# Optimization experiments

Measured on AMD Instinct MI355X. Metric: run time of the kernel, lower is better.

Reference implementation:

```python
import jax, jax.numpy as jnp
import numpy as np

N_NODES = 50000
N_EDGES = 800000
C_IN = 64
N_HEADS = 4
HEAD_DIM = 16
FC = 64


def setup_inputs() -> dict:
    key = jax.random.key(0)
    ks = jax.random.split(key, 20)
    d = {}
    d["node_input"] = jax.random.normal(ks[0], (N_NODES, C_IN), jnp.float32)
    d["node_attr"] = jnp.ones((N_NODES, 1), jnp.float32)
    d["edge_src"] = jax.random.randint(ks[1], (N_EDGES,), 0, N_NODES)
    d["edge_dst"] = jax.random.randint(ks[2], (N_EDGES,), 0, N_NODES)
    d["edge_attr"] = jax.random.normal(ks[3], (N_EDGES, 1), jnp.float32)
    d["edge_scalars"] = jax.random.normal(ks[4], (N_EDGES, FC), jnp.float32)
    d["batch"] = jnp.zeros((N_NODES,), jnp.int32)
    s = 1.0 / np.sqrt(C_IN)
    AD = N_HEADS * HEAD_DIM  # 64
    d["Wq"] = jax.random.normal(ks[5], (C_IN, AD), jnp.float32) * s
    d["bq"] = jnp.zeros((AD,), jnp.float32)
    d["W_src"] = jax.random.normal(ks[6], (C_IN, C_IN), jnp.float32) * s
    d["b_src"] = jnp.zeros((C_IN,), jnp.float32)
    d["W_dst"] = jax.random.normal(ks[7], (C_IN, C_IN), jnp.float32) * s
    d["W_fc1"] = jax.random.normal(ks[8], (FC, FC), jnp.float32) * (1.0 / np.sqrt(FC))
    d["b_fc1"] = jnp.zeros((FC,), jnp.float32)
    d["W_fc2"] = jax.random.normal(ks[9], (FC, FC), jnp.float32) * (1.0 / np.sqrt(FC))
    d["b_fc2"] = jnp.zeros((FC,), jnp.float32)
    d["W_fc3"] = jax.random.normal(ks[10], (FC, C_IN), jnp.float32) * (1.0 / np.sqrt(FC))
    d["b_fc3"] = jnp.zeros((C_IN,), jnp.float32)
    d["W_kv"] = jax.random.normal(ks[11], (C_IN, 2 * AD), jnp.float32) * s
    d["b_kv"] = jnp.zeros((2 * AD,), jnp.float32)
    d["W_proj"] = jax.random.normal(ks[12], (AD, C_IN), jnp.float32) * (1.0 / np.sqrt(AD))
    d["b_proj"] = jnp.zeros((C_IN,), jnp.float32)
    return d


def reference(node_input, node_attr, edge_src, edge_dst, edge_attr, edge_scalars, batch,
              Wq, bq, W_src, b_src, W_dst, W_fc1, b_fc1, W_fc2, b_fc2, W_fc3, b_fc3,
              W_kv, b_kv, W_proj, b_proj):
    N = node_input.shape[0]
    # query: linear -> heads -> scale (ScaleFactor for HxH 0e irreps = 1/sqrt(num_irreps))
    q = (node_input @ Wq + bq).reshape(N, N_HEADS, HEAD_DIM)
    q = q * (1.0 / jnp.sqrt(jnp.float32(HEAD_DIM)))
    # edge messages
    msg_src = node_input @ W_src + b_src
    msg_dst = node_input @ W_dst
    kv = msg_src[edge_src] + msg_dst[edge_dst]  # [E, C]
    # SeparableFCTP (scalar irreps): radial MLP -> depthwise weights, x * edge_attr, linear
    h = jax.nn.silu(edge_scalars @ W_fc1 + b_fc1)
    h = jax.nn.silu(h @ W_fc2 + b_fc2)
    w = h @ W_fc3 + b_fc3  # [E, C] depthwise TP weights
    tp = kv * edge_attr * w
    kv2 = (tp @ W_kv + b_kv).reshape(-1, 2 * N_HEADS, HEAD_DIM)
    k = kv2[:, :N_HEADS]
    v = kv2[:, N_HEADS:]
    # per-edge scores and segment softmax over incoming edges of each dst node
    alpha = jnp.einsum('ehd,ehd->eh', q[edge_dst], k)  # [E, H]
    seg_max = jax.ops.segment_max(alpha, edge_dst, num_segments=N)
    seg_max = jnp.where(jnp.isfinite(seg_max), seg_max, 0.0)
    ex = jnp.exp(alpha - seg_max[edge_dst])
    denom = jax.ops.segment_sum(ex, edge_dst, num_segments=N)
    alpha = ex / (denom[edge_dst] + 1e-16)
    # weighted scatter-sum of values
    attn = jax.ops.segment_sum(v * alpha[..., None], edge_dst, num_segments=N)
    attn = attn.reshape(N, N_HEADS * HEAD_DIM)
    return attn @ W_proj + b_proj
```

## Files before the change

### kernel.cpp

```cpp
#include <hip/hip_runtime.h>
#include <hip/hip_bf16.h>


typedef __attribute__((ext_vector_type(8))) short    bf16x8;
typedef __attribute__((ext_vector_type(4))) float    f32x4;
typedef __attribute__((ext_vector_type(4))) unsigned short ushort4v;

__device__ __forceinline__ unsigned short f2bf(float x) {
    union { float f; unsigned u; } v; v.f = x;
    unsigned r = v.u + 0x7fffu + ((v.u >> 16) & 1u);
    return (unsigned short)(r >> 16);
}

__device__ __forceinline__ int swz(int row, int k) {
    return row * 64 + (k ^ ((row & 7) << 3));
}

__device__ __forceinline__ bf16x8 ldfrag(const unsigned short* buf, int rn, int kk, int lhi) {
    return *(const bf16x8*)(buf + swz(rn, kk * 32 + lhi * 8));
}

__global__ __launch_bounds__(256)
void prep_weights(const float* __restrict__ W1, const float* __restrict__ W2,
                  const float* __restrict__ W3, const float* __restrict__ Wkv,
                  unsigned short* __restrict__ wbf)
{
    const int d = blockIdx.x * 256 + threadIdx.x;
    if (d < 12288) {
        const int w  = d >> 12;
        const int r  = d & 4095;
        const int n  = r >> 6, kx = r & 63;
        const int k  = kx ^ ((n & 7) << 3);
        const float* W = (w == 0) ? W1 : (w == 1) ? W2 : W3;
        wbf[d] = f2bf(W[k * 64 + n]);
    } else if (d < 20480) {
        const int r  = d - 12288;
        const int n  = r >> 6, kx = r & 63;
        const int k  = kx ^ ((n & 7) << 3);
        wbf[d] = f2bf(Wkv[k * 128 + n]);
    }
}

__global__ __launch_bounds__(384)
void node_linear_kernel(const float* __restrict__ x,
                        const float* __restrict__ Wq,   const float* __restrict__ bq,
                        const float* __restrict__ Wsrc, const float* __restrict__ bsrc,
                        const float* __restrict__ Wdst,
                        float* __restrict__ qout, float* __restrict__ msout,
                        float* __restrict__ mdout, int N, int ntiles)
{
    __shared__ __align__(16) float sW[64 * 192];
    __shared__ float sb[192];
    __shared__ __align__(16) float xs[32][68];

    const int t = threadIdx.x;
    for (int idx4 = t; idx4 < 3072; idx4 += 384) {
        const int k  = idx4 / 48;
        const int j4 = idx4 % 48;
        const float4* src = (j4 < 16) ? (const float4*)&Wq  [k * 64 + j4 * 4]
                         : (j4 < 32) ? (const float4*)&Wsrc[k * 64 + (j4 - 16) * 4]
                                     : (const float4*)&Wdst[k * 64 + (j4 - 32) * 4];
        ((float4*)sW)[idx4] = *src;
    }
    if (t < 192) sb[t] = (t < 64) ? bq[t] : (t < 128) ? bsrc[t - 64] : 0.0f;

    const int te = t / 48, tj = t % 48;
    const int j0 = tj * 4, e0 = te * 4;

    for (int tile = blockIdx.x; tile < ntiles; tile += gridDim.x) {
        const int nbase = tile * 32;
        __syncthreads();
        for (int idx = t; idx < 512; idx += 384) {
            const int n  = idx >> 4;
            const int c4 = (idx & 15) * 4;
            const int gn = nbase + n;
            float4 g = make_float4(0.f, 0.f, 0.f, 0.f);
            if (gn < N) g = *(const float4*)&x[(size_t)gn * 64 + c4];
            *(float4*)&xs[n][c4] = g;
        }
        __syncthreads();

        float acc[4][4];
#pragma unroll
        for (int i = 0; i < 4; ++i)
#pragma unroll
            for (int c = 0; c < 4; ++c) acc[i][c] = 0.f;

#pragma unroll 16
        for (int k = 0; k < 64; ++k) {
            const float4 wv = *(const float4*)&sW[k * 192 + j0];
            const float a0 = xs[e0 + 0][k], a1 = xs[e0 + 1][k];
            const float a2 = xs[e0 + 2][k], a3 = xs[e0 + 3][k];
            acc[0][0] += a0 * wv.x; acc[0][1] += a0 * wv.y; acc[0][2] += a0 * wv.z; acc[0][3] += a0 * wv.w;
            acc[1][0] += a1 * wv.x; acc[1][1] += a1 * wv.y; acc[1][2] += a1 * wv.z; acc[1][3] += a1 * wv.w;
            acc[2][0] += a2 * wv.x; acc[2][1] += a2 * wv.y; acc[2][2] += a2 * wv.z; acc[2][3] += a2 * wv.w;
            acc[3][0] += a3 * wv.x; acc[3][1] += a3 * wv.y; acc[3][2] += a3 * wv.z; acc[3][3] += a3 * wv.w;
        }

#pragma unroll
        for (int i = 0; i < 4; ++i) {
            const int gn = nbase + e0 + i;
            if (gn >= N) continue;
            float4 o;
            o.x = acc[i][0] + sb[j0 + 0];
            o.y = acc[i][1] + sb[j0 + 1];
            o.z = acc[i][2] + sb[j0 + 2];
            o.w = acc[i][3] + sb[j0 + 3];
            if (j0 < 64) {
                o.x *= 0.25f; o.y *= 0.25f; o.z *= 0.25f; o.w *= 0.25f;
                *(float4*)&qout[(size_t)gn * 64 + j0] = o;
            } else if (j0 < 128) {
                *(float4*)&msout[(size_t)gn * 64 + (j0 - 64)] = o;
            } else {
                *(float4*)&mdout[(size_t)gn * 64 + (j0 - 128)] = o;
            }
        }
    }
}

__global__ __launch_bounds__(512, 4)
void edge_fused_mfma(const int* __restrict__ esrc, const int* __restrict__ edst,
                     const float* __restrict__ eattr, const float* __restrict__ escal,
                     const unsigned short* __restrict__ wbf,
                     const float* __restrict__ b1, const float* __restrict__ b2,
                     const float* __restrict__ b3, const float* __restrict__ bkv,
                     const float* __restrict__ qbuf, const float* __restrict__ msrc,
                     const float* __restrict__ mdst,
                     float* __restrict__ num, float* __restrict__ den, int ntiles)
{
    __shared__ __align__(16) unsigned short sh[36864];
    unsigned short* sW1t  = sh;
    unsigned short* sW2t  = sh + 4096;
    unsigned short* sW3t  = sh + 8192;
    unsigned short* sWkvt = sh + 12288;
    unsigned short* sA0   = sh + 20480;
    unsigned short* sA1   = sh + 28672;
    __shared__ float sB1[64], sB2[64], sB3[64], sBkv[128], sEa[128];
    __shared__ int   sSrc[128], sDst[128];

    const int t    = threadIdx.x;
    const int lane = t & 63;
    const int wave = t >> 6;
    const int l15  = lane & 15;
    const int lhi  = lane >> 4;
    const int rowBase = wave * 16;

    for (int i4 = t; i4 < 2560; i4 += 512)
        ((float4*)sh)[i4] = ((const float4*)wbf)[i4];
    if (t < 64)              { sB1[t] = b1[t]; sB2[t] = b2[t]; sB3[t] = b3[t]; }
    if (t >= 64 && t < 192)  sBkv[t - 64] = bkv[t - 64];

    for (int tile = blockIdx.x; tile < ntiles; tile += gridDim.x) {
        const int base = tile * 128;
        __syncthreads();

        {
            int e = t >> 4;
            const int c4 = (t & 15) << 2;
#pragma unroll
            for (int p = 0; p < 4; ++p, e += 32) {
                const float4 g = *(const float4*)&escal[(size_t)(base + e) * 64 + c4];
                ushort4v pk = { f2bf(g.x), f2bf(g.y), f2bf(g.z), f2bf(g.w) };
                *(ushort4v*)&sA0[swz(e, c4)] = pk;
            }
        }
        if (t >= 192 && t < 320) {
            const int e = t - 192;
            sSrc[e] = esrc[base + e];
            sDst[e] = edst[base + e];
            sEa[e]  = eattr[base + e];
        }
        __syncthreads();

        {
            f32x4 acc[4] = {{0,0,0,0},{0,0,0,0},{0,0,0,0},{0,0,0,0}};
#pragma unroll
            for (int kk = 0; kk < 2; ++kk) {
                const bf16x8 a = ldfrag(sA0, rowBase + l15, kk, lhi);
#pragma unroll
                for (int c = 0; c < 4; ++c) {
                    const bf16x8 b = ldfrag(sW1t, c * 16 + l15, kk, lhi);
                    acc[c] = __builtin_amdgcn_mfma_f32_16x16x32_bf16(a, b, acc[c], 0, 0, 0);
                }
            }
#pragma unroll
            for (int c = 0; c < 4; ++c)
#pragma unroll
                for (int r = 0; r < 4; ++r) {
                    const int row = rowBase + lhi * 4 + r;
                    const int col = c * 16 + l15;
                    const float v = acc[c][r] + sB1[col];
                    sA1[swz(row, col)] = f2bf(v / (1.f + __expf(-v)));
                }
        }
        __syncthreads();

        {
            f32x4 acc[4] = {{0,0,0,0},{0,0,0,0},{0,0,0,0},{0,0,0,0}};
#pragma unroll
            for (int kk = 0; kk < 2; ++kk) {
                const bf16x8 a = ldfrag(sA1, rowBase + l15, kk, lhi);
#pragma unroll
                for (int c = 0; c < 4; ++c) {
                    const bf16x8 b = ldfrag(sW2t, c * 16 + l15, kk, lhi);
                    acc[c] = __builtin_amdgcn_mfma_f32_16x16x32_bf16(a, b, acc[c], 0, 0, 0);
                }
            }
#pragma unroll
            for (int c = 0; c < 4; ++c)
#pragma unroll
                for (int r = 0; r < 4; ++r) {
                    const int row = rowBase + lhi * 4 + r;
                    const int col = c * 16 + l15;
                    const float v = acc[c][r] + sB2[col];
                    sA0[swz(row, col)] = f2bf(v / (1.f + __expf(-v)));
                }
        }
        __syncthreads();

        {
            f32x4 acc[4] = {{0,0,0,0},{0,0,0,0},{0,0,0,0},{0,0,0,0}};
#pragma unroll
            for (int kk = 0; kk < 2; ++kk) {
                const bf16x8 a = ldfrag(sA0, rowBase + l15, kk, lhi);
#pragma unroll
                for (int c = 0; c < 4; ++c) {
                    const bf16x8 b = ldfrag(sW3t, c * 16 + l15, kk, lhi);
                    acc[c] = __builtin_amdgcn_mfma_f32_16x16x32_bf16(a, b, acc[c], 0, 0, 0);
                }
            }
            float ms[4][4], md[4][4];
#pragma unroll
            for (int c = 0; c < 4; ++c)
#pragma unroll
                for (int r = 0; r < 4; ++r) {
                    const int row = rowBase + lhi * 4 + r;
                    const int col = c * 16 + l15;
                    ms[c][r] = msrc[(size_t)sSrc[row] * 64 + col];
                    md[c][r] = mdst[(size_t)sDst[row] * 64 + col];
                }
#pragma unroll
            for (int c = 0; c < 4; ++c)
#pragma unroll
                for (int r = 0; r < 4; ++r) {
                    const int row = rowBase + lhi * 4 + r;
                    const int col = c * 16 + l15;
                    const float w  = acc[c][r] + sB3[col];
                    const float tp = (ms[c][r] + md[c][r]) * sEa[row] * w;
                    sA1[swz(row, col)] = f2bf(tp);
                }
        }
        __syncthreads();

        f32x4 acc2[8] = {{0,0,0,0},{0,0,0,0},{0,0,0,0},{0,0,0,0},
                         {0,0,0,0},{0,0,0,0},{0,0,0,0},{0,0,0,0}};
#pragma unroll
        for (int kk = 0; kk < 2; ++kk) {
            const bf16x8 a = ldfrag(sA1, rowBase + l15, kk, lhi);
#pragma unroll
            for (int c = 0; c < 8; ++c) {
                const bf16x8 b = ldfrag(sWkvt, c * 16 + l15, kk, lhi);
                acc2[c] = __builtin_amdgcn_mfma_f32_16x16x32_bf16(a, b, acc2[c], 0, 0, 0);
            }
        }

        int   gds[4];
        float qreg[4][4];
#pragma unroll
        for (int r = 0; r < 4; ++r) gds[r] = sDst[rowBase + lhi * 4 + r];
#pragma unroll
        for (int h = 0; h < 4; ++h)
#pragma unroll
            for (int r = 0; r < 4; ++r)
                qreg[h][r] = qbuf[(size_t)gds[r] * 64 + h * 16 + l15];

        float ex[4][4];
#pragma unroll
        for (int h = 0; h < 4; ++h)
#pragma unroll
            for (int r = 0; r < 4; ++r) {
                float s = (acc2[h][r] + sBkv[h * 16 + l15]) * qreg[h][r];
                s += __shfl_xor(s, 1);
                s += __shfl_xor(s, 2);
                s += __shfl_xor(s, 4);
                s += __shfl_xor(s, 8);
                const float e = __expf(s);
                ex[h][r] = e;
                if (l15 == h * 4 + r) atomicAdd(&den[(size_t)gds[r] * 4 + h], e);
            }

#pragma unroll
        for (int vt = 0; vt < 4; ++vt)
#pragma unroll
            for (int r = 0; r < 4; ++r) {
                const float vv = acc2[4 + vt][r] + sBkv[64 + vt * 16 + l15];
                atomicAdd(&num[(size_t)gds[r] * 64 + vt * 16 + l15], ex[vt][r] * vv);
            }
    }
}

__global__ __launch_bounds__(256)
void final_proj_kernel(const float* __restrict__ num, const float* __restrict__ den,
                       const float* __restrict__ Wp, const float* __restrict__ bp,
                       float* __restrict__ out, int N, int ntiles)
{
    __shared__ __align__(16) float sW[64 * 64];
    __shared__ float sb[64];
    __shared__ __align__(16) float at[64][68];

    const int t = threadIdx.x;
    for (int i4 = t; i4 < 1024; i4 += 256)
        ((float4*)sW)[i4] = ((const float4*)Wp)[i4];
    if (t < 64) sb[t] = bp[t];

    const int te = t >> 4, tj = t & 15;
    const int j0 = tj * 4, e0 = te * 4;

    for (int tile = blockIdx.x; tile < ntiles; tile += gridDim.x) {
        const int nbase = tile * 64;
        __syncthreads();
        for (int idx = t; idx < 1024; idx += 256) {
            const int n  = idx >> 4;
            const int c4 = (idx & 15) * 4;
            const int gn = nbase + n;
            float4 g = make_float4(0.f, 0.f, 0.f, 0.f);
            if (gn < N) {
                const float4 nm = *(const float4*)&num[(size_t)gn * 64 + c4];
                const float inv = 1.0f / (den[(size_t)gn * 4 + (c4 >> 4)] + 1e-16f);
                g = make_float4(nm.x * inv, nm.y * inv, nm.z * inv, nm.w * inv);
            }
            *(float4*)&at[n][c4] = g;
        }
        __syncthreads();

        float acc[4][4];
#pragma unroll
        for (int i = 0; i < 4; ++i)
#pragma unroll
            for (int c = 0; c < 4; ++c) acc[i][c] = 0.f;

#pragma unroll 16
        for (int k = 0; k < 64; ++k) {
            const float4 wv = *(const float4*)&sW[k * 64 + j0];
            const float a0 = at[e0 + 0][k], a1 = at[e0 + 1][k];
            const float a2 = at[e0 + 2][k], a3 = at[e0 + 3][k];
            acc[0][0] += a0 * wv.x; acc[0][1] += a0 * wv.y; acc[0][2] += a0 * wv.z; acc[0][3] += a0 * wv.w;
            acc[1][0] += a1 * wv.x; acc[1][1] += a1 * wv.y; acc[1][2] += a1 * wv.z; acc[1][3] += a1 * wv.w;
            acc[2][0] += a2 * wv.x; acc[2][1] += a2 * wv.y; acc[2][2] += a2 * wv.z; acc[2][3] += a2 * wv.w;
            acc[3][0] += a3 * wv.x; acc[3][1] += a3 * wv.y; acc[3][2] += a3 * wv.z; acc[3][3] += a3 * wv.w;
        }

#pragma unroll
        for (int i = 0; i < 4; ++i) {
            const int gn = nbase + e0 + i;
            if (gn >= N) continue;
            float4 o;
            o.x = acc[i][0] + sb[j0 + 0];
            o.y = acc[i][1] + sb[j0 + 1];
            o.z = acc[i][2] + sb[j0 + 2];
            o.w = acc[i][3] + sb[j0 + 3];
            *(float4*)&out[(size_t)gn * 64 + j0] = o;
        }
    }
}

extern "C" void kernel_launch(void* const* d_in, const int* in_sizes, int n_in,
                              void* d_out, int out_size, void* d_ws, size_t ws_size,
                              hipStream_t stream)
{
    const float* node_input = (const float*)d_in[0];
    const int*   edge_src   = (const int*)  d_in[2];
    const int*   edge_dst   = (const int*)  d_in[3];
    const float* edge_attr  = (const float*)d_in[4];
    const float* edge_scal  = (const float*)d_in[5];
    const float* Wq    = (const float*)d_in[7];
    const float* bq    = (const float*)d_in[8];
    const float* W_src = (const float*)d_in[9];
    const float* b_src = (const float*)d_in[10];
    const float* W_dst = (const float*)d_in[11];
    const float* W_fc1 = (const float*)d_in[12];
    const float* b_fc1 = (const float*)d_in[13];
    const float* W_fc2 = (const float*)d_in[14];
    const float* b_fc2 = (const float*)d_in[15];
    const float* W_fc3 = (const float*)d_in[16];
    const float* b_fc3 = (const float*)d_in[17];
    const float* W_kv  = (const float*)d_in[18];
    const float* b_kv  = (const float*)d_in[19];
    const float* W_proj = (const float*)d_in[20];
    const float* b_proj = (const float*)d_in[21];

    const int N = in_sizes[0] / 64;
    const int E = in_sizes[2];

    float* ws    = (float*)d_ws;
    float* q_buf = ws;
    float* msrc  = ws + (size_t)N * 64;
    float* mdst  = ws + (size_t)N * 128;
    float* num   = ws + (size_t)N * 192;
    float* den   = ws + (size_t)N * 256;
    unsigned short* wbf = (unsigned short*)(ws + (size_t)N * 260);

    hipMemsetAsync(num, 0, (size_t)N * 68 * sizeof(float), stream);

    prep_weights<<<80, 256, 0, stream>>>(W_fc1, W_fc2, W_fc3, W_kv, wbf);

    {
        const int ntiles = (N + 31) / 32;
        node_linear_kernel<<<512, 384, 0, stream>>>(node_input, Wq, bq, W_src, b_src, W_dst,
                                                    q_buf, msrc, mdst, N, ntiles);
    }
    {
        const int ntiles = E / 128;
        edge_fused_mfma<<<512, 512, 0, stream>>>(edge_src, edge_dst, edge_attr, edge_scal,
                                                 wbf, b_fc1, b_fc2, b_fc3, b_kv,
                                                 q_buf, msrc, mdst, num, den, ntiles);
    }
    {
        const int ntiles = (N + 63) / 64;
        final_proj_kernel<<<512, 256, 0, stream>>>(num, den, W_proj, b_proj,
                                                   (float*)d_out, N, ntiles);
    }
}
```

Baseline: 672.2 us.

## Make edge tiles wave-private, drop block barriers, and prefetch query gathers

```diff
diff --git a/kernel.cpp b/kernel.cpp
--- a/kernel.cpp
+++ b/kernel.cpp
@@ -19,6 +19,8 @@
 __device__ __forceinline__ bf16x8 ldfrag(const unsigned short* buf, int rn, int kk, int lhi) {
     return *(const bf16x8*)(buf + swz(rn, kk * 32 + lhi * 8));
 }
+
+#define PHASE_FENCE() asm volatile("" ::: "memory")
 
 __global__ __launch_bounds__(256)
 void prep_weights(const float* __restrict__ W1, const float* __restrict__ W2,
@@ -135,8 +137,7 @@
     unsigned short* sWkvt = sh + 12288;
     unsigned short* sA0   = sh + 20480;
     unsigned short* sA1   = sh + 28672;
-    __shared__ float sB1[64], sB2[64], sB3[64], sBkv[128], sEa[128];
-    __shared__ int   sSrc[128], sDst[128];
+    __shared__ float sB1[64], sB2[64], sB3[64], sBkv[128];
 
     const int t    = threadIdx.x;
     const int lane = t & 63;
@@ -144,33 +145,46 @@
     const int l15  = lane & 15;
     const int lhi  = lane >> 4;
     const int rowBase = wave * 16;
+    const int r4   = lhi * 4;
 
     for (int i4 = t; i4 < 2560; i4 += 512)
         ((float4*)sh)[i4] = ((const float4*)wbf)[i4];
     if (t < 64)              { sB1[t] = b1[t]; sB2[t] = b2[t]; sB3[t] = b3[t]; }
     if (t >= 64 && t < 192)  sBkv[t - 64] = bkv[t - 64];
+    __syncthreads();
+
+    const int srow = lane >> 4;
+    const int scol = (lane & 15) << 2;
 
     for (int tile = blockIdx.x; tile < ntiles; tile += gridDim.x) {
-        const int base = tile * 128;
-        __syncthreads();
-
-        {
-            int e = t >> 4;
-            const int c4 = (t & 15) << 2;
-#pragma unroll
-            for (int p = 0; p < 4; ++p, e += 32) {
-                const float4 g = *(const float4*)&escal[(size_t)(base + e) * 64 + c4];
-                ushort4v pk = { f2bf(g.x), f2bf(g.y), f2bf(g.z), f2bf(g.w) };
-                *(ushort4v*)&sA0[swz(e, c4)] = pk;
-            }
-        }
-        if (t >= 192 && t < 320) {
-            const int e = t - 192;
-            sSrc[e] = esrc[base + e];
-            sDst[e] = edst[base + e];
-            sEa[e]  = eattr[base + e];
-        }
-        __syncthreads();
+        const int base  = tile * 128;
+        const int ebase = base + rowBase;
+
+#pragma unroll
+        for (int p = 0; p < 4; ++p) {
+            const int row = p * 4 + srow;
+            const float4 g = *(const float4*)&escal[(size_t)(ebase + row) * 64 + scol];
+            ushort4v pk = { f2bf(g.x), f2bf(g.y), f2bf(g.z), f2bf(g.w) };
+            *(ushort4v*)&sA0[swz(rowBase + row, scol)] = pk;
+        }
+
+        int   gsrc[4], gdst[4];
+        float gea[4];
+#pragma unroll
+        for (int r = 0; r < 4; ++r) {
+            const int e = ebase + r4 + r;
+            gsrc[r] = esrc[e];
+            gdst[r] = edst[e];
+            gea[r]  = eattr[e];
+        }
+        float qreg[4][4];
+#pragma unroll
+        for (int h = 0; h < 4; ++h)
+#pragma unroll
+            for (int r = 0; r < 4; ++r)
+                qreg[h][r] = qbuf[(size_t)gdst[r] * 64 + h * 16 + l15];
+
+        PHASE_FENCE();
 
         {
             f32x4 acc[4] = {{0,0,0,0},{0,0,0,0},{0,0,0,0},{0,0,0,0}};
@@ -187,13 +201,13 @@
             for (int c = 0; c < 4; ++c)
 #pragma unroll
                 for (int r = 0; r < 4; ++r) {
-                    const int row = rowBase + lhi * 4 + r;
+                    const int row = rowBase + r4 + r;
                     const int col = c * 16 + l15;
                     const float v = acc[c][r] + sB1[col];
                     sA1[swz(row, col)] = f2bf(v / (1.f + __expf(-v)));
                 }
         }
-        __syncthreads();
+        PHASE_FENCE();
 
         {
             f32x4 acc[4] = {{0,0,0,0},{0,0,0,0},{0,0,0,0},{0,0,0,0}};
@@ -210,13 +224,13 @@
             for (int c = 0; c < 4; ++c)
 #pragma unroll
                 for (int r = 0; r < 4; ++r) {
-                    const int row = rowBase + lhi * 4 + r;
+                    const int row = rowBase + r4 + r;
                     const int col = c * 16 + l15;
                     const float v = acc[c][r] + sB2[col];
                     sA0[swz(row, col)] = f2bf(v / (1.f + __expf(-v)));
                 }
         }
-        __syncthreads();
+        PHASE_FENCE();
 
         {
             f32x4 acc[4] = {{0,0,0,0},{0,0,0,0},{0,0,0,0},{0,0,0,0}};
@@ -234,23 +248,22 @@
             for (int c = 0; c < 4; ++c)
 #pragma unroll
                 for (int r = 0; r < 4; ++r) {
-                    const int row = rowBase + lhi * 4 + r;
                     const int col = c * 16 + l15;
-                    ms[c][r] = msrc[(size_t)sSrc[row] * 64 + col];
-                    md[c][r] = mdst[(size_t)sDst[row] * 64 + col];
+                    ms[c][r] = msrc[(size_t)gsrc[r] * 64 + col];
+                    md[c][r] = mdst[(size_t)gdst[r] * 64 + col];
                 }
 #pragma unroll
             for (int c = 0; c < 4; ++c)
 #pragma unroll
                 for (int r = 0; r < 4; ++r) {
-                    const int row = rowBase + lhi * 4 + r;
+                    const int row = rowBase + r4 + r;
                     const int col = c * 16 + l15;
                     const float w  = acc[c][r] + sB3[col];
-                    const float tp = (ms[c][r] + md[c][r]) * sEa[row] * w;
+                    const float tp = (ms[c][r] + md[c][r]) * gea[r] * w;
                     sA1[swz(row, col)] = f2bf(tp);
                 }
         }
-        __syncthreads();
+        PHASE_FENCE();
 
         f32x4 acc2[8] = {{0,0,0,0},{0,0,0,0},{0,0,0,0},{0,0,0,0},
                          {0,0,0,0},{0,0,0,0},{0,0,0,0},{0,0,0,0}};
@@ -263,16 +276,6 @@
                 acc2[c] = __builtin_amdgcn_mfma_f32_16x16x32_bf16(a, b, acc2[c], 0, 0, 0);
             }
         }
-
-        int   gds[4];
-        float qreg[4][4];
-#pragma unroll
-        for (int r = 0; r < 4; ++r) gds[r] = sDst[rowBase + lhi * 4 + r];
-#pragma unroll
-        for (int h = 0; h < 4; ++h)
-#pragma unroll
-            for (int r = 0; r < 4; ++r)
-                qreg[h][r] = qbuf[(size_t)gds[r] * 64 + h * 16 + l15];
 
         float ex[4][4];
 #pragma unroll
@@ -286,7 +289,7 @@
                 s += __shfl_xor(s, 8);
                 const float e = __expf(s);
                 ex[h][r] = e;
-                if (l15 == h * 4 + r) atomicAdd(&den[(size_t)gds[r] * 4 + h], e);
+                if (l15 == h * 4 + r) atomicAdd(&den[(size_t)gdst[r] * 4 + h], e);
             }
 
 #pragma unroll
@@ -294,8 +297,10 @@
 #pragma unroll
             for (int r = 0; r < 4; ++r) {
                 const float vv = acc2[4 + vt][r] + sBkv[64 + vt * 16 + l15];
-                atomicAdd(&num[(size_t)gds[r] * 64 + vt * 16 + l15], ex[vt][r] * vv);
-            }
+                atomicAdd(&num[(size_t)gdst[r] * 64 + vt * 16 + l15], ex[vt][r] * vv);
+            }
+
+        PHASE_FENCE();
     }
 }
 
```

Result: no change. 672.0 us (-0.0%).
